# Performance work log

Hardware: AMD Instinct MI355X
Metric: run time of the kernel (lower is better)

The kernel has to match this reference:

```python
import jax, jax.numpy as jnp
import numpy as np

B, NQ, NK = 4, 2048, 2048
DQ = DK = DV = 512
H = 8
DS = DV // H  # 64


def _layernorm(x, g, b, eps=1e-5):
    m = jnp.mean(x, axis=-1, keepdims=True)
    v = jnp.var(x, axis=-1, keepdims=True)
    return (x - m) * jax.lax.rsqrt(v + eps) * g + b


def setup_inputs() -> dict:
    key = jax.random.key(0)
    ks = jax.random.split(key, 16)
    def lin(k, fan_in, fan_out):
        # torch nn.Linear default init: U(-1/sqrt(fan_in), 1/sqrt(fan_in))
        bound = 1.0 / np.sqrt(fan_in)
        k1, k2 = jax.random.split(k)
        W = jax.random.uniform(k1, (fan_in, fan_out), jnp.float32, -bound, bound)
        b = jax.random.uniform(k2, (fan_out,), jnp.float32, -bound, bound)
        return W, b
    Wq, bq = lin(ks[0], DQ, DV)
    Wk, bk = lin(ks[1], DK, DV)
    Wv, bv = lin(ks[2], DK, DV)
    W0, b0 = lin(ks[3], DV, DV)
    W1, b1 = lin(ks[4], DV, DV)
    # xavier_uniform for kp/vp of shape (1, DS): bound = sqrt(6/(1+DS))
    xb = np.sqrt(6.0 / (1 + DS))
    kp = jax.random.uniform(ks[5], (DS,), jnp.float32, -xb, xb)
    vp = jax.random.uniform(ks[6], (DS,), jnp.float32, -xb, xb)
    return {
        "Q": jax.random.normal(ks[7], (B, NQ, DQ), jnp.float32),
        "K": jax.random.normal(ks[8], (B, NK, DK), jnp.float32),
        "Kpos": jax.random.uniform(ks[9], (B, NQ, NK), jnp.float32),
        "Wq": Wq, "bq": bq, "Wk": Wk, "bk": bk, "Wv": Wv, "bv": bv,
        "kp": kp, "vp": vp,
        "W0": W0, "b0": b0, "W1": W1, "b1": b1,
        "g0": jnp.ones((DV,), jnp.float32), "be0": jnp.zeros((DV,), jnp.float32),
        "g1": jnp.ones((DV,), jnp.float32), "be1": jnp.zeros((DV,), jnp.float32),
    }


def reference(Q, K, Kpos, Wq, bq, Wk, bk, Wv, bv, kp, vp, W0, b0, W1, b1, g0, be0, g1, be1):
    Qp = Q @ Wq + bq                       # [B,NQ,DV]
    Kp = K @ Wk + bk                       # [B,NK,DV]
    Vp = K @ Wv + bv                       # [B,NK,DV]
    # head split (torch split/cat along batch == reshape to [B,N,H,DS])
    Qh = Qp.reshape(B, NQ, H, DS)
    Kh = Kp.reshape(B, NK, H, DS)
    Vh = Vp.reshape(B, NK, H, DS)
    scale = 1.0 / np.sqrt(DV)              # NOTE: original scales by sqrt(dim_V), not per-head dim
    scores = jnp.einsum('bqhd,bkhd->bhqk', Qh, Kh) * scale
    # ShawRE key bias: KE[b,h,q,k] = Kpos[b,q,k] * <Qh[b,q,h,:], kp>
    qkp = jnp.einsum('bqhd,d->bhq', Qh, kp)          # [B,H,NQ]
    scores = scores + Kpos[:, None, :, :] * qkp[:, :, :, None]
    A = jax.nn.softmax(scores, axis=-1)              # [B,H,NQ,NK]
    out = jnp.einsum('bhqk,bkhd->bqhd', A, Vh)       # [B,NQ,H,DS]
    # ShawRE value bias: VE[b,q,h,:] = (sum_k A*Kpos) * vp
    akp = jnp.einsum('bhqk,bqk->bhq', A, Kpos)       # [B,H,NQ]
    out = out + akp.transpose(0, 2, 1)[..., None] * vp
    O = (Qh + out).reshape(B, NQ, DV)
    O = _layernorm(O, g0, be0)
    resO = O
    O = jax.nn.relu(O @ W0 + b0)           # fc_o[0] with relu (numlayers=2)
    O = resO + jax.nn.relu(O @ W1 + b1)    # fc_o[-1] + residual
    O = _layernorm(O, g1, be1)
    return O
```

## Files before the change

kernel.cpp:

```cpp
#include <hip/hip_runtime.h>
#include <math.h>

#define Bx  4
#define NQx 2048
#define NKx 2048
#define Dx  512
#define Hx  8

typedef __attribute__((ext_vector_type(8))) __bf16 bf16x8;
typedef __attribute__((ext_vector_type(4))) float f32x4;
typedef __attribute__((ext_vector_type(16))) float f32x16;

typedef const __attribute__((address_space(1))) unsigned int* gas_ptr;
typedef __attribute__((address_space(3))) unsigned int* lds_ptr;

__device__ __forceinline__ void gload16(const void* g, void* l){
  __builtin_amdgcn_global_load_lds((gas_ptr)g, (lds_ptr)l, 16, 0, 0);
}

__device__ __forceinline__ unsigned short f2bf(float f){
  union { float f; unsigned int u; } v; v.f = f;
  unsigned int r = (v.u + 0x7FFFu + ((v.u >> 16) & 1u)) >> 16;
  return (unsigned short)r;
}
__device__ __forceinline__ float bf2f(unsigned short u){
  union { unsigned int u; float f; } v; v.u = ((unsigned int)u) << 16; return v.f;
}
__device__ __forceinline__ unsigned int cvtpk_bf16(float a, float b){
  unsigned int d;
  asm("v_cvt_pk_bf16_f32 %0, %1, %2" : "=v"(d) : "v"(a), "v"(b));
  return d;
}
__device__ __forceinline__ void plane32_swap(unsigned int& a, unsigned int& b){
  asm("v_permlane32_swap_b32 %0, %1" : "+v"(a), "+v"(b));
}
__device__ __forceinline__ float fexp2(float x){
  float d; asm("v_exp_f32 %0, %1" : "=v"(d) : "v"(x)); return d;
}
__device__ __forceinline__ float fmax3(float a, float b, float c){
  float d; asm("v_max3_f32 %0, %1, %2, %3" : "=v"(d) : "v"(a), "v"(b), "v"(c)); return d;
}

__global__ __launch_bounds__(256) void mab_wt(
    const float* __restrict__ Wq, const float* __restrict__ Wk, const float* __restrict__ Wv,
    const float* __restrict__ W0, const float* __restrict__ W1,
    unsigned short* __restrict__ Wt)
{
  __shared__ unsigned short T[64][72];
  const int z = blockIdx.z;
  const float* W = (z==0)?Wq:(z==1)?Wk:(z==2)?Wv:(z==3)?W0:W1;
  unsigned short* O = Wt + (size_t)z*512*512;
  const int k0 = blockIdx.x*64, n0 = blockIdx.y*64;
  const int tid = threadIdx.x;
  #pragma unroll
  for (int i=0;i<4;++i){
    int id = tid + i*256;
    int r = id>>4, c4 = id&15;
    float4 v = *(const float4*)(W + (size_t)(k0+r)*512 + n0 + c4*4);
    ushort4 o; o.x=f2bf(v.x); o.y=f2bf(v.y); o.z=f2bf(v.z); o.w=f2bf(v.w);
    *(ushort4*)&T[r][c4*4] = o;
  }
  __syncthreads();
  #pragma unroll
  for (int i=0;i<2;++i){
    int id = tid + i*256;
    int c = id>>3, r8 = id&7;
    union { unsigned short u[8]; uint4 v; } o;
    #pragma unroll
    for (int j=0;j<8;++j) o.u[j] = T[r8*8+j][c];
    *(uint4*)(O + (size_t)(n0+c)*512 + k0 + r8*8) = o.v;
  }
}

__global__ __launch_bounds__(256) void mab_vt(
    const unsigned short* __restrict__ Vp, unsigned short* __restrict__ Vpt)
{
  __shared__ unsigned short T[64][72];
  const int r0 = blockIdx.x*64;
  const int c0 = blockIdx.y*64;
  const int b  = blockIdx.z;
  const int tid = threadIdx.x;
  #pragma unroll
  for (int i=0;i<2;++i){
    int id = tid + i*256;
    int r = id>>3, c8 = id&7;
    *(uint4*)&T[r][c8*8] = *(const uint4*)(Vp + (size_t)(b*NKx + r0+r)*512 + c0 + c8*8);
  }
  __syncthreads();
  #pragma unroll
  for (int i=0;i<2;++i){
    int id = tid + i*256;
    int c = id>>3, r8 = id&7;
    union { unsigned short u[8]; uint4 v; } o;
    #pragma unroll
    for (int j=0;j<8;++j) o.u[j] = T[r8*8+j][c];
    *(uint4*)(Vpt + ((size_t)(b*512) + c0 + c)*NKx + r0 + r8*8) = o.v;
  }
}

__global__ __launch_bounds__(256) void mab_gemm_proj(
    const float* __restrict__ Qf, const float* __restrict__ Kf,
    const unsigned short* __restrict__ Wt,
    const float* __restrict__ bq, const float* __restrict__ bk, const float* __restrict__ bv,
    unsigned short* __restrict__ Cb, float kscale)
{
  __shared__ unsigned short As[128][64];
  __shared__ unsigned short Bs[128][64];
  const int z = blockIdx.z;
  const float* A = (z==0) ? Qf : Kf;
  const unsigned short* W = Wt + (size_t)z*512*512;
  const float* bias = (z==0)?bq:((z==1)?bk:bv);
  const float sc = (z==1) ? kscale : 1.0f;
  const int m0 = blockIdx.y*128, n0 = blockIdx.x*128;
  const int tid = threadIdx.x, w = tid>>6, lane = tid&63, g = lane>>4, q16 = lane&15;
  const int wr = w>>1, wc = w&1;

  f32x4 acc[4][4];
  #pragma unroll
  for (int m=0;m<4;++m)
    #pragma unroll
    for (int n=0;n<4;++n) acc[m][n] = (f32x4){0.f,0.f,0.f,0.f};

  float4 areg[8];
  #pragma unroll
  for (int i=0;i<8;++i){
    int id = i*256 + tid, row = id>>4, qc = id&15;
    areg[i] = *(const float4*)(A + (size_t)(m0+row)*512 + qc*4);
  }

  for (int k0 = 0; k0 < 512; k0 += 64){
    __syncthreads();
    #pragma unroll
    for (int i=0;i<8;++i){
      int id = i*256 + tid, row = id>>4, qc = id&15;
      unsigned int lo = cvtpk_bf16(areg[i].x, areg[i].y);
      unsigned int hi = cvtpk_bf16(areg[i].z, areg[i].w);
      unsigned int* dst = (unsigned int*)((char*)&As[0][0] + row*128
                          + ((qc>>1) ^ (row&7))*16 + (qc&1)*8);
      dst[0] = lo; dst[1] = hi;
    }
    #pragma unroll
    for (int i=0;i<4;++i){
      int o   = (w*4 + i)*1024 + lane*16;
      int row = o >> 7;
      int c   = (o >> 4) & 7;
      int cs  = c ^ (row & 7);
      gload16(W + (size_t)(n0+row)*512 + k0 + cs*8, (char*)&Bs[0][0] + (w*4+i)*1024);
    }
    __syncthreads();
    if (k0 + 64 < 512){
      #pragma unroll
      for (int i=0;i<8;++i){
        int id = i*256 + tid, row = id>>4, qc = id&15;
        areg[i] = *(const float4*)(A + (size_t)(m0+row)*512 + (k0+64) + qc*4);
      }
    }
    #pragma unroll
    for (int ks=0;ks<2;++ks){
      bf16x8 af[4], bfr[4];
      #pragma unroll
      for (int m=0;m<4;++m){
        int row = wr*64 + m*16 + q16;
        int c   = (ks*4 + g) ^ (row & 7);
        af[m] = *(const bf16x8*)((const char*)&As[0][0] + row*128 + c*16);
      }
      #pragma unroll
      for (int n=0;n<4;++n){
        int row = wc*64 + n*16 + q16;
        int c   = (ks*4 + g) ^ (row & 7);
        bfr[n] = *(const bf16x8*)((const char*)&Bs[0][0] + row*128 + c*16);
      }
      #pragma unroll
      for (int m=0;m<4;++m)
        #pragma unroll
        for (int n=0;n<4;++n)
          acc[m][n] = __builtin_amdgcn_mfma_f32_16x16x32_bf16(af[m], bfr[n], acc[m][n], 0,0,0);
    }
  }

  const size_t ZS = (size_t)8192*512;
  #pragma unroll
  for (int m=0;m<4;++m){
    const int rowl = wr*64 + m*16 + g*4;
    #pragma unroll
    for (int n=0;n<4;++n){
      const int col = n0 + wc*64 + n*16 + q16;
      const float bv2 = bias[col];
      #pragma unroll
      for (int r=0;r<4;++r){
        float v = (acc[m][n][r] + bv2) * sc;
        Cb[(size_t)z*ZS + (size_t)(m0 + rowl + r)*512 + col] = f2bf(v);
      }
    }
  }
}

__global__ __launch_bounds__(256) void mab_gemm_mfma(
    const unsigned short* __restrict__ A, const unsigned short* __restrict__ W,
    const float* __restrict__ bias, const float* __restrict__ res,
    unsigned short* __restrict__ Cb, float* __restrict__ Cf, int relu)
{
  __shared__ unsigned short As[128][64];
  __shared__ unsigned short Bs[128][64];
  const int m0 = blockIdx.y*128, n0 = blockIdx.x*128;
  const int tid = threadIdx.x, w = tid>>6, lane = tid&63, g = lane>>4, q16 = lane&15;
  const int wr = w>>1, wc = w&1;

  f32x4 acc[4][4];
  #pragma unroll
  for (int m=0;m<4;++m)
    #pragma unroll
    for (int n=0;n<4;++n) acc[m][n] = (f32x4){0.f,0.f,0.f,0.f};

  for (int k0 = 0; k0 < 512; k0 += 64){
    __syncthreads();
    #pragma unroll
    for (int i=0;i<4;++i){
      int o   = (w*4 + i)*1024 + lane*16;
      int row = o >> 7;
      int c   = (o >> 4) & 7;
      int cs  = c ^ (row & 7);
      gload16(A + (size_t)(m0+row)*512 + k0 + cs*8, (char*)&As[0][0] + (w*4+i)*1024);
      gload16(W + (size_t)(n0+row)*512 + k0 + cs*8, (char*)&Bs[0][0] + (w*4+i)*1024);
    }
    __syncthreads();
    #pragma unroll
    for (int ks=0;ks<2;++ks){
      bf16x8 af[4], bfr[4];
      #pragma unroll
      for (int m=0;m<4;++m){
        int row = wr*64 + m*16 + q16;
        int c   = (ks*4 + g) ^ (row & 7);
        af[m] = *(const bf16x8*)((const char*)&As[0][0] + row*128 + c*16);
      }
      #pragma unroll
      for (int n=0;n<4;++n){
        int row = wc*64 + n*16 + q16;
        int c   = (ks*4 + g) ^ (row & 7);
        bfr[n] = *(const bf16x8*)((const char*)&Bs[0][0] + row*128 + c*16);
      }
      #pragma unroll
      for (int m=0;m<4;++m)
        #pragma unroll
        for (int n=0;n<4;++n)
          acc[m][n] = __builtin_amdgcn_mfma_f32_16x16x32_bf16(af[m], bfr[n], acc[m][n], 0,0,0);
    }
  }

  #pragma unroll
  for (int m=0;m<4;++m){
    const int rowl = wr*64 + m*16 + g*4;
    #pragma unroll
    for (int n=0;n<4;++n){
      const int col = n0 + wc*64 + n*16 + q16;
      const float bv = bias[col];
      #pragma unroll
      for (int r=0;r<4;++r){
        float v = acc[m][n][r] + bv;
        if (relu) v = fmaxf(v, 0.f);
        size_t off = (size_t)(m0 + rowl + r)*512 + col;
        if (res) v += res[off];
        if (Cb) Cb[off] = f2bf(v);
        if (Cf) Cf[off] = v;
      }
    }
  }
}

__global__ __launch_bounds__(256) void mab_attn2(
    const unsigned short* __restrict__ Qp, const unsigned short* __restrict__ Kp,
    const unsigned short* __restrict__ Vpt,
    const float* __restrict__ Kpos, const float* __restrict__ kp, const float* __restrict__ vp,
    float* __restrict__ X)
{
  __shared__ unsigned short Kb[2][64][64];
  __shared__ unsigned short Vb[2][64][64];
  __shared__ unsigned short Qs[128][72];

  const int q0 = blockIdx.x*128;
  const int h  = blockIdx.y;
  const int b  = blockIdx.z;
  const int tid = threadIdx.x, w = tid>>6, lane = tid&63;
  const int q32 = lane & 31, hi = lane >> 5;

  const unsigned short* Qg = Qp + ((size_t)(b*NQx + q0))*Dx + h*64;
  const unsigned short* Kg = Kp + ((size_t)b*NKx)*Dx + h*64;
  const unsigned short* Vg = Vpt + ((size_t)(b*512) + h*64)*NKx;
  const float* KProw = Kpos + (size_t)b*NQx*NKx + (size_t)(q0 + w*32 + q32)*NKx;

  const int sr = lane>>3;
  const int sc = lane&7;

  #pragma unroll
  for (int i=0;i<2;++i){
    int r  = i*8 + sr;
    int cs = sc ^ (r & 7);
    gload16(Kg + (size_t)(w*16 + r)*Dx + cs*8, (char*)&Kb[0][0][0] + w*2048 + i*1024);
    gload16(Vg + (size_t)(w*16 + r)*NKx + cs*8, (char*)&Vb[0][0][0] + w*2048 + i*1024);
  }
  f32x4 kq[2][4];
  #pragma unroll
  for (int n=0;n<2;++n)
    #pragma unroll
    for (int a=0;a<4;++a)
      kq[n][a] = *(const f32x4*)(KProw + n*32 + a*8 + hi*4);
  #pragma unroll
  for (int i=0;i<4;++i){
    int id = tid + i*256;
    int r = id>>3, c8 = id&7;
    *(uint4*)&Qs[r][c8*8] = *(const uint4*)(Qg + (size_t)r*Dx + c8*8);
  }
  __syncthreads();

  bf16x8 qf[4];
  #pragma unroll
  for (int ds=0; ds<4; ++ds)
    qf[ds] = *(const bf16x8*)&Qs[w*32 + q32][ds*16 + hi*8];

  float qkp = 0.f;
  #pragma unroll
  for (int ds=0; ds<4; ++ds){
    union { bf16x8 v; unsigned short u[8]; } qa; qa.v = qf[ds];
    #pragma unroll
    for (int j=0;j<8;++j)
      qkp = fmaf(bf2f(qa.u[j]), kp[ds*16 + hi*8 + j], qkp);
  }
  qkp += __shfl_xor(qkp, 32);
  qkp *= 1.4426950408889634f;

  float m_i = -1e30f, l_i = 0.f, a_i = 0.f;
  f32x16 accT[2];
  #pragma unroll
  for (int db=0; db<2; ++db)
    #pragma unroll
    for (int r=0;r<16;++r) accT[db][r] = 0.f;

  const int NT = NKx/64;

  for (int kt = 0; kt < NT; ++kt){
    const int cur = kt & 1;
    const int k0 = kt*64;

    if (kt+1 < NT){
      const int k1 = k0 + 64;
      #pragma unroll
      for (int i=0;i<2;++i){
        int r  = i*8 + sr;
        int cs = sc ^ (r & 7);
        gload16(Kg + (size_t)(k1 + w*16 + r)*Dx + cs*8,
                (char*)&Kb[cur^1][0][0] + w*2048 + i*1024);
        gload16(Vg + (size_t)(w*16 + r)*NKx + k1 + cs*8,
                (char*)&Vb[cur^1][0][0] + w*2048 + i*1024);
      }
    }
    __builtin_amdgcn_sched_barrier(0);

    f32x16 sT[2];
    __builtin_amdgcn_s_setprio(1);
    #pragma unroll
    for (int n=0;n<2;++n){
      f32x16 c;
      #pragma unroll
      for (int r=0;r<16;++r) c[r] = 0.f;
      #pragma unroll
      for (int ds=0; ds<4; ++ds){
        int row = n*32 + q32;
        int cc  = (ds*2 + hi) ^ (q32 & 7);
        bf16x8 kf = *(const bf16x8*)((const char*)&Kb[cur][0][0] + row*128 + cc*16);
        c = __builtin_amdgcn_mfma_f32_32x32x16_bf16(kf, qf[ds], c, 0,0,0);
      }
      sT[n] = c;
    }
    __builtin_amdgcn_s_setprio(0);

    #pragma unroll
    for (int n=0;n<2;++n)
      #pragma unroll
      for (int r=0;r<16;++r)
        sT[n][r] = fmaf(kq[n][r>>2][r&3], qkp, sT[n][r]);

    float m0a = fmax3(sT[0][0], sT[0][1], sT[0][2]);
    float m0b = fmax3(sT[0][3], sT[0][4], sT[0][5]);
    float m0c = fmax3(sT[0][6], sT[0][7], sT[0][8]);
    float m0d = fmax3(sT[0][9], sT[0][10], sT[0][11]);
    float m0e = fmax3(sT[0][12], sT[0][13], sT[0][14]);
    float m1a = fmax3(sT[1][0], sT[1][1], sT[1][2]);
    float m1b = fmax3(sT[1][3], sT[1][4], sT[1][5]);
    float m1c = fmax3(sT[1][6], sT[1][7], sT[1][8]);
    float m1d = fmax3(sT[1][9], sT[1][10], sT[1][11]);
    float m1e = fmax3(sT[1][12], sT[1][13], sT[1][14]);
    float rm = fmax3(fmax3(m0a, m0b, m0c), fmax3(m0d, m0e, sT[0][15]),
                     fmax3(fmax3(m1a, m1b, m1c), fmax3(m1d, m1e, sT[1][15]), m_i));
    rm = fmaxf(rm, __shfl_xor(rm, 32));

    if (!__all(rm <= m_i + 11.544f)){
      float al = fexp2(m_i - rm);
      m_i = rm;
      l_i *= al; a_i *= al;
      #pragma unroll
      for (int db=0; db<2; ++db)
        #pragma unroll
        for (int r=0;r<16;++r) accT[db][r] *= al;
    }

    float ps = 0.f, pk = 0.f;
    #pragma unroll
    for (int n=0;n<2;++n)
      #pragma unroll
      for (int r=0;r<16;++r){
        float p = fexp2(sT[n][r] - m_i);
        sT[n][r] = p;
        ps += p;
        pk = fmaf(p, kq[n][r>>2][r&3], pk);
      }

    {
      const int kn = (kt+1 < NT) ? (k0 + 64) : k0;
      #pragma unroll
      for (int n=0;n<2;++n)
        #pragma unroll
        for (int a=0;a<4;++a)
          kq[n][a] = *(const f32x4*)(KProw + kn + n*32 + a*8 + hi*4);
    }

    ps += __shfl_xor(ps, 32);
    pk += __shfl_xor(pk, 32);
    l_i += ps; a_i += pk;

    union PW { unsigned int u[4]; bf16x8 v; } pa[4];
    #pragma unroll
    for (int n=0;n<2;++n){
      unsigned int w0 = cvtpk_bf16(sT[n][0],  sT[n][1]);
      unsigned int w1 = cvtpk_bf16(sT[n][2],  sT[n][3]);
      unsigned int w2 = cvtpk_bf16(sT[n][4],  sT[n][5]);
      unsigned int w3 = cvtpk_bf16(sT[n][6],  sT[n][7]);
      unsigned int w4 = cvtpk_bf16(sT[n][8],  sT[n][9]);
      unsigned int w5 = cvtpk_bf16(sT[n][10], sT[n][11]);
      unsigned int w6 = cvtpk_bf16(sT[n][12], sT[n][13]);
      unsigned int w7 = cvtpk_bf16(sT[n][14], sT[n][15]);
      plane32_swap(w0, w2);
      plane32_swap(w1, w3);
      plane32_swap(w4, w6);
      plane32_swap(w5, w7);
      pa[n*2+0].u[0]=w0; pa[n*2+0].u[1]=w1; pa[n*2+0].u[2]=w2; pa[n*2+0].u[3]=w3;
      pa[n*2+1].u[0]=w4; pa[n*2+1].u[1]=w5; pa[n*2+1].u[2]=w6; pa[n*2+1].u[3]=w7;
    }

    __builtin_amdgcn_s_setprio(1);
    #pragma unroll
    for (int st=0; st<4; ++st){
      #pragma unroll
      for (int db=0; db<2; ++db){
        int row = db*32 + q32;
        int cc  = (st*2 + hi) ^ (q32 & 7);
        bf16x8 vf = *(const bf16x8*)((const char*)&Vb[cur][0][0] + row*128 + cc*16);
        accT[db] = __builtin_amdgcn_mfma_f32_32x32x16_bf16(vf, pa[st].v, accT[db], 0,0,0);
      }
    }
    __builtin_amdgcn_s_setprio(0);

    asm volatile("s_waitcnt vmcnt(8)" ::: "memory");
    __builtin_amdgcn_s_barrier();
  }

  float inv = 1.0f / l_i;
  float aw  = a_i * inv;
  float* Xrow = X + ((size_t)(b*NQx + q0 + w*32 + q32))*Dx + h*64;
  #pragma unroll
  for (int db=0; db<2; ++db){
    #pragma unroll
    for (int a=0; a<4; ++a){
      int d0 = db*32 + a*8 + hi*4;
      f32x4 vpv = *(const f32x4*)(vp + d0);
      float4 o;
      o.x = fmaf(accT[db][a*4+0], inv, bf2f(Qs[w*32+q32][d0+0]) + aw*vpv[0]);
      o.y = fmaf(accT[db][a*4+1], inv, bf2f(Qs[w*32+q32][d0+1]) + aw*vpv[1]);
      o.z = fmaf(accT[db][a*4+2], inv, bf2f(Qs[w*32+q32][d0+2]) + aw*vpv[2]);
      o.w = fmaf(accT[db][a*4+3], inv, bf2f(Qs[w*32+q32][d0+3]) + aw*vpv[3]);
      *(float4*)(Xrow + d0) = o;
    }
  }
}

__global__ __launch_bounds__(256) void mab_ln2(
    const float* __restrict__ Xin, const float* __restrict__ g,
    const float* __restrict__ be, float* __restrict__ Yf, unsigned short* __restrict__ Yb)
{
  const int row = blockIdx.x;
  const int tid = threadIdx.x;
  const float* x = Xin + (size_t)row*Dx;
  float2 v = *(const float2*)(x + tid*2);
  float s  = v.x + v.y;
  float sq = fmaf(v.x,v.x, v.y*v.y);
  #pragma unroll
  for (int m=1; m<64; m<<=1){ s += __shfl_xor(s,m); sq += __shfl_xor(sq,m); }
  __shared__ float red[2][4];
  const int wid = tid>>6, lane = tid&63;
  if (lane==0){ red[0][wid]=s; red[1][wid]=sq; }
  __syncthreads();
  s  = red[0][0]+red[0][1]+red[0][2]+red[0][3];
  sq = red[1][0]+red[1][1]+red[1][2]+red[1][3];
  float mean = s*(1.0f/Dx);
  float var  = sq*(1.0f/Dx) - mean*mean;
  float rstd = rsqrtf(var + 1e-5f);
  float2 gg = *(const float2*)(g  + tid*2);
  float2 bb = *(const float2*)(be + tid*2);
  float2 o;
  o.x = (v.x-mean)*rstd*gg.x + bb.x;
  o.y = (v.y-mean)*rstd*gg.y + bb.y;
  if (Yf) *(float2*)(Yf + (size_t)row*Dx + tid*2) = o;
  if (Yb){
    ushort2 ob; ob.x = f2bf(o.x); ob.y = f2bf(o.y);
    *(ushort2*)(Yb + (size_t)row*Dx + tid*2) = ob;
  }
}

extern "C" void kernel_launch(void* const* d_in, const int* in_sizes, int n_in,
                              void* d_out, int out_size, void* d_ws, size_t ws_size,
                              hipStream_t stream)
{
  const float* Q    = (const float*)d_in[0];
  const float* K    = (const float*)d_in[1];
  const float* Kpos = (const float*)d_in[2];
  const float* Wq   = (const float*)d_in[3];
  const float* bq   = (const float*)d_in[4];
  const float* Wk   = (const float*)d_in[5];
  const float* bk   = (const float*)d_in[6];
  const float* Wv   = (const float*)d_in[7];
  const float* bv   = (const float*)d_in[8];
  const float* kp   = (const float*)d_in[9];
  const float* vp   = (const float*)d_in[10];
  const float* W0   = (const float*)d_in[11];
  const float* b0   = (const float*)d_in[12];
  const float* W1   = (const float*)d_in[13];
  const float* b1   = (const float*)d_in[14];
  const float* g0   = (const float*)d_in[15];
  const float* be0  = (const float*)d_in[16];
  const float* g1   = (const float*)d_in[17];
  const float* be1  = (const float*)d_in[18];
  float* out = (float*)d_out;
  char* wsb  = (char*)d_ws;

  const size_t MB = 1024*1024;
  unsigned short* Qp  = (unsigned short*)(wsb);
  unsigned short* Kp  = (unsigned short*)(wsb + 8*MB);
  unsigned short* Vp  = (unsigned short*)(wsb + 16*MB);
  float*          O0  = (float*)         (wsb + 24*MB);
  unsigned short* Vpt = (unsigned short*)(wsb + 40*MB);
  unsigned short* O0b = (unsigned short*)(wsb + 48*MB);
  unsigned short* Wt  = (unsigned short*)(wsb + 56*MB);
  unsigned short* T1  = Vp;

  const float kscale = 0.044194173824159216f * 1.4426950408889634f;

  mab_wt<<<dim3(8,8,5), 256, 0, stream>>>(Wq, Wk, Wv, W0, W1, Wt);
  mab_gemm_proj<<<dim3(4,64,3), 256, 0, stream>>>(Q, K, Wt, bq, bk, bv, Qp, kscale);
  mab_vt<<<dim3(32,8,4), 256, 0, stream>>>(Vp, Vpt);
  mab_attn2<<<dim3(16,8,4), 256, 0, stream>>>(Qp, Kp, Vpt, Kpos, kp, vp, out);
  mab_ln2<<<8192, 256, 0, stream>>>(out, g0, be0, O0, O0b);
  mab_gemm_mfma<<<dim3(4,64,1), 256, 0, stream>>>(
      O0b, Wt + (size_t)3*512*512, b0, nullptr, T1, nullptr, 1);
  mab_gemm_mfma<<<dim3(4,64,1), 256, 0, stream>>>(
      T1, Wt + (size_t)4*512*512, b1, O0, nullptr, out, 1);
  mab_ln2<<<8192, 256, 0, stream>>>(out, g1, be1, out, nullptr);
}
```

Before: 210.0 us.

## Split attention over key halves and merge partials inside the first layernorm

The attention kernel now splits the key range into two halves across the grid's z dimension, doubling the block count from 512 to 1024. Each block writes unnormalized bf16 partial outputs plus its running max, sum and Kpos-weighted sum. A new merge kernel combines the halves, adds the Q residual and vp bias, and applies the first layernorm, writing only bf16. Other changes: Q is read straight from global memory instead of through LDS, the Kpos loads move to the top of each iteration, occupancy is hinted at 4 blocks, and the residual is read back as bf16. This adds traffic for the partial results and the merge pass, and a bf16 residual loses precision.

```diff
diff --git a/kernel.cpp b/kernel.cpp
--- a/kernel.cpp
+++ b/kernel.cpp
@@ -197,7 +197,7 @@
 
 __global__ __launch_bounds__(256) void mab_gemm_mfma(
     const unsigned short* __restrict__ A, const unsigned short* __restrict__ W,
-    const float* __restrict__ bias, const float* __restrict__ res,
+    const float* __restrict__ bias, const unsigned short* __restrict__ resb,
     unsigned short* __restrict__ Cb, float* __restrict__ Cf, int relu)
 {
   __shared__ unsigned short As[128][64];
@@ -259,7 +259,7 @@
         float v = acc[m][n][r] + bv;
         if (relu) v = fmaxf(v, 0.f);
         size_t off = (size_t)(m0 + rowl + r)*512 + col;
-        if (res) v += res[off];
+        if (resb) v += bf2f(resb[off]);
         if (Cb) Cb[off] = f2bf(v);
         if (Cf) Cf[off] = v;
       }
@@ -267,23 +267,23 @@
   }
 }
 
-__global__ __launch_bounds__(256) void mab_attn2(
+__global__ __launch_bounds__(256, 4) void mab_attn6(
     const unsigned short* __restrict__ Qp, const unsigned short* __restrict__ Kp,
     const unsigned short* __restrict__ Vpt,
-    const float* __restrict__ Kpos, const float* __restrict__ kp, const float* __restrict__ vp,
-    float* __restrict__ X)
+    const float* __restrict__ Kpos, const float* __restrict__ kp,
+    unsigned short* __restrict__ OP, float4* __restrict__ MLA)
 {
   __shared__ unsigned short Kb[2][64][64];
   __shared__ unsigned short Vb[2][64][64];
-  __shared__ unsigned short Qs[128][72];
 
   const int q0 = blockIdx.x*128;
   const int h  = blockIdx.y;
-  const int b  = blockIdx.z;
+  const int b  = blockIdx.z >> 1;
+  const int zz = blockIdx.z & 1;
   const int tid = threadIdx.x, w = tid>>6, lane = tid&63;
   const int q32 = lane & 31, hi = lane >> 5;
-
-  const unsigned short* Qg = Qp + ((size_t)(b*NQx + q0))*Dx + h*64;
+  const int kbase = zz*1024;
+
   const unsigned short* Kg = Kp + ((size_t)b*NKx)*Dx + h*64;
   const unsigned short* Vg = Vpt + ((size_t)(b*512) + h*64)*NKx;
   const float* KProw = Kpos + (size_t)b*NQx*NKx + (size_t)(q0 + w*32 + q32)*NKx;
@@ -293,29 +293,17 @@
 
   #pragma unroll
   for (int i=0;i<2;++i){
-    int r  = i*8 + sr;
+    int r  = w*16 + i*8 + sr;
     int cs = sc ^ (r & 7);
-    gload16(Kg + (size_t)(w*16 + r)*Dx + cs*8, (char*)&Kb[0][0][0] + w*2048 + i*1024);
-    gload16(Vg + (size_t)(w*16 + r)*NKx + cs*8, (char*)&Vb[0][0][0] + w*2048 + i*1024);
-  }
-  f32x4 kq[2][4];
-  #pragma unroll
-  for (int n=0;n<2;++n)
-    #pragma unroll
-    for (int a=0;a<4;++a)
-      kq[n][a] = *(const f32x4*)(KProw + n*32 + a*8 + hi*4);
-  #pragma unroll
-  for (int i=0;i<4;++i){
-    int id = tid + i*256;
-    int r = id>>3, c8 = id&7;
-    *(uint4*)&Qs[r][c8*8] = *(const uint4*)(Qg + (size_t)r*Dx + c8*8);
-  }
-  __syncthreads();
-
+    gload16(Kg + (size_t)(kbase + r)*Dx + cs*8, (char*)&Kb[0][0][0] + w*2048 + i*1024);
+    gload16(Vg + (size_t)r*NKx + kbase + cs*8, (char*)&Vb[0][0][0] + w*2048 + i*1024);
+  }
+
+  const unsigned short* Qrowp = Qp + ((size_t)(b*NQx + q0 + w*32 + q32))*Dx + h*64;
   bf16x8 qf[4];
   #pragma unroll
   for (int ds=0; ds<4; ++ds)
-    qf[ds] = *(const bf16x8*)&Qs[w*32 + q32][ds*16 + hi*8];
+    qf[ds] = *(const bf16x8*)(Qrowp + ds*16 + hi*8);
 
   float qkp = 0.f;
   #pragma unroll
@@ -335,21 +323,28 @@
     #pragma unroll
     for (int r=0;r<16;++r) accT[db][r] = 0.f;
 
-  const int NT = NKx/64;
-
-  for (int kt = 0; kt < NT; ++kt){
-    const int cur = kt & 1;
-    const int k0 = kt*64;
-
-    if (kt+1 < NT){
+  __syncthreads();
+
+  for (int t = 0; t < 16; ++t){
+    const int cur = t & 1;
+    const int k0 = kbase + t*64;
+
+    f32x4 kq[2][4];
+    #pragma unroll
+    for (int n=0;n<2;++n)
+      #pragma unroll
+      for (int a=0;a<4;++a)
+        kq[n][a] = *(const f32x4*)(KProw + k0 + n*32 + a*8 + hi*4);
+
+    if (t+1 < 16){
       const int k1 = k0 + 64;
       #pragma unroll
       for (int i=0;i<2;++i){
-        int r  = i*8 + sr;
+        int r  = w*16 + i*8 + sr;
         int cs = sc ^ (r & 7);
-        gload16(Kg + (size_t)(k1 + w*16 + r)*Dx + cs*8,
+        gload16(Kg + (size_t)(k1 + r)*Dx + cs*8,
                 (char*)&Kb[cur^1][0][0] + w*2048 + i*1024);
-        gload16(Vg + (size_t)(w*16 + r)*NKx + k1 + cs*8,
+        gload16(Vg + (size_t)r*NKx + k1 + cs*8,
                 (char*)&Vb[cur^1][0][0] + w*2048 + i*1024);
       }
     }
@@ -413,16 +408,6 @@
         ps += p;
         pk = fmaf(p, kq[n][r>>2][r&3], pk);
       }
-
-    {
-      const int kn = (kt+1 < NT) ? (k0 + 64) : k0;
-      #pragma unroll
-      for (int n=0;n<2;++n)
-        #pragma unroll
-        for (int a=0;a<4;++a)
-          kq[n][a] = *(const f32x4*)(KProw + kn + n*32 + a*8 + hi*4);
-    }
-
     ps += __shfl_xor(ps, 32);
     pk += __shfl_xor(pk, 32);
     l_i += ps; a_i += pk;
@@ -459,32 +444,80 @@
     }
     __builtin_amdgcn_s_setprio(0);
 
-    asm volatile("s_waitcnt vmcnt(8)" ::: "memory");
-    __builtin_amdgcn_s_barrier();
-  }
-
-  float inv = 1.0f / l_i;
-  float aw  = a_i * inv;
-  float* Xrow = X + ((size_t)(b*NQx + q0 + w*32 + q32))*Dx + h*64;
+    __syncthreads();
+  }
+
+  const size_t rowg = (size_t)(b*NQx + q0 + w*32 + q32);
+  unsigned short* Orow = OP + (size_t)zz*(8192*512) + rowg*Dx + h*64;
   #pragma unroll
   for (int db=0; db<2; ++db){
     #pragma unroll
-    for (int a=0; a<4; ++a){
-      int d0 = db*32 + a*8 + hi*4;
-      f32x4 vpv = *(const f32x4*)(vp + d0);
-      float4 o;
-      o.x = fmaf(accT[db][a*4+0], inv, bf2f(Qs[w*32+q32][d0+0]) + aw*vpv[0]);
-      o.y = fmaf(accT[db][a*4+1], inv, bf2f(Qs[w*32+q32][d0+1]) + aw*vpv[1]);
-      o.z = fmaf(accT[db][a*4+2], inv, bf2f(Qs[w*32+q32][d0+2]) + aw*vpv[2]);
-      o.w = fmaf(accT[db][a*4+3], inv, bf2f(Qs[w*32+q32][d0+3]) + aw*vpv[3]);
-      *(float4*)(Xrow + d0) = o;
-    }
-  }
+    for (int a2=0; a2<4; ++a2){
+      int d0 = db*32 + a2*8 + hi*4;
+      uint2 pk2;
+      pk2.x = cvtpk_bf16(accT[db][a2*4+0], accT[db][a2*4+1]);
+      pk2.y = cvtpk_bf16(accT[db][a2*4+2], accT[db][a2*4+3]);
+      *(uint2*)(Orow + d0) = pk2;
+    }
+  }
+  if (hi == 0){
+    float4 mla; mla.x = m_i; mla.y = l_i; mla.z = a_i; mla.w = 0.f;
+    MLA[(size_t)zz*65536 + rowg*8 + h] = mla;
+  }
+}
+
+__global__ __launch_bounds__(256) void mab_merge_ln(
+    const unsigned short* __restrict__ OP, const float4* __restrict__ MLA,
+    const unsigned short* __restrict__ Qp, const float* __restrict__ vp,
+    const float* __restrict__ g, const float* __restrict__ be,
+    unsigned short* __restrict__ Yb)
+{
+  const int row = blockIdx.x;
+  const int tid = threadIdx.x;
+  const int h = tid >> 5;
+  const size_t R = (size_t)8192*512;
+
+  float4 A0 = MLA[(size_t)row*8 + h];
+  float4 A1 = MLA[65536 + (size_t)row*8 + h];
+  float mM  = fmaxf(A0.x, A1.x);
+  float al0 = fexp2(A0.x - mM), al1 = fexp2(A1.x - mM);
+  float l   = fmaf(al0, A0.y, al1*A1.y);
+  float inv = 1.0f / l;
+  float aw  = fmaf(al0, A0.z, al1*A1.z) * inv;
+
+  const int d = tid*2;
+  ushort2 o0 = *(const ushort2*)(OP + (size_t)row*Dx + d);
+  ushort2 o1 = *(const ushort2*)(OP + R + (size_t)row*Dx + d);
+  ushort2 qh = *(const ushort2*)(Qp + (size_t)row*Dx + d);
+  float2 vv  = *(const float2*)(vp + (d & 63));
+  float2 v;
+  v.x = fmaf(fmaf(al0, bf2f(o0.x), al1*bf2f(o1.x)), inv, bf2f(qh.x) + aw*vv.x);
+  v.y = fmaf(fmaf(al0, bf2f(o0.y), al1*bf2f(o1.y)), inv, bf2f(qh.y) + aw*vv.y);
+
+  float s  = v.x + v.y;
+  float sq = fmaf(v.x,v.x, v.y*v.y);
+  #pragma unroll
+  for (int m=1; m<64; m<<=1){ s += __shfl_xor(s,m); sq += __shfl_xor(sq,m); }
+  __shared__ float red[2][4];
+  const int wid = tid>>6, lane = tid&63;
+  if (lane==0){ red[0][wid]=s; red[1][wid]=sq; }
+  __syncthreads();
+  s  = red[0][0]+red[0][1]+red[0][2]+red[0][3];
+  sq = red[1][0]+red[1][1]+red[1][2]+red[1][3];
+  float mean = s*(1.0f/Dx);
+  float var  = sq*(1.0f/Dx) - mean*mean;
+  float rstd = rsqrtf(var + 1e-5f);
+  float2 gg = *(const float2*)(g  + d);
+  float2 bb = *(const float2*)(be + d);
+  ushort2 ob;
+  ob.x = f2bf((v.x-mean)*rstd*gg.x + bb.x);
+  ob.y = f2bf((v.y-mean)*rstd*gg.y + bb.y);
+  *(ushort2*)(Yb + (size_t)row*Dx + d) = ob;
 }
 
 __global__ __launch_bounds__(256) void mab_ln2(
     const float* __restrict__ Xin, const float* __restrict__ g,
-    const float* __restrict__ be, float* __restrict__ Yf, unsigned short* __restrict__ Yb)
+    const float* __restrict__ be, float* __restrict__ Yf)
 {
   const int row = blockIdx.x;
   const int tid = threadIdx.x;
@@ -508,11 +541,7 @@
   float2 o;
   o.x = (v.x-mean)*rstd*gg.x + bb.x;
   o.y = (v.y-mean)*rstd*gg.y + bb.y;
-  if (Yf) *(float2*)(Yf + (size_t)row*Dx + tid*2) = o;
-  if (Yb){
-    ushort2 ob; ob.x = f2bf(o.x); ob.y = f2bf(o.y);
-    *(ushort2*)(Yb + (size_t)row*Dx + tid*2) = ob;
-  }
+  *(float2*)(Yf + (size_t)row*Dx + tid*2) = o;
 }
 
 extern "C" void kernel_launch(void* const* d_in, const int* in_sizes, int n_in,
@@ -545,10 +574,11 @@
   unsigned short* Qp  = (unsigned short*)(wsb);
   unsigned short* Kp  = (unsigned short*)(wsb + 8*MB);
   unsigned short* Vp  = (unsigned short*)(wsb + 16*MB);
-  float*          O0  = (float*)         (wsb + 24*MB);
-  unsigned short* Vpt = (unsigned short*)(wsb + 40*MB);
-  unsigned short* O0b = (unsigned short*)(wsb + 48*MB);
-  unsigned short* Wt  = (unsigned short*)(wsb + 56*MB);
+  unsigned short* Vpt = (unsigned short*)(wsb + 24*MB);
+  unsigned short* OP  = (unsigned short*)(wsb + 32*MB);
+  float4*         MLA = (float4*)        (wsb + 48*MB);
+  unsigned short* Wt  = (unsigned short*)(wsb + 50*MB);
+  unsigned short* O0b = Vpt;
   unsigned short* T1  = Vp;
 
   const float kscale = 0.044194173824159216f * 1.4426950408889634f;
@@ -556,11 +586,11 @@
   mab_wt<<<dim3(8,8,5), 256, 0, stream>>>(Wq, Wk, Wv, W0, W1, Wt);
   mab_gemm_proj<<<dim3(4,64,3), 256, 0, stream>>>(Q, K, Wt, bq, bk, bv, Qp, kscale);
   mab_vt<<<dim3(32,8,4), 256, 0, stream>>>(Vp, Vpt);
-  mab_attn2<<<dim3(16,8,4), 256, 0, stream>>>(Qp, Kp, Vpt, Kpos, kp, vp, out);
-  mab_ln2<<<8192, 256, 0, stream>>>(out, g0, be0, O0, O0b);
+  mab_attn6<<<dim3(16,8,8), 256, 0, stream>>>(Qp, Kp, Vpt, Kpos, kp, OP, MLA);
+  mab_merge_ln<<<8192, 256, 0, stream>>>(OP, MLA, Qp, vp, g0, be0, O0b);
   mab_gemm_mfma<<<dim3(4,64,1), 256, 0, stream>>>(
       O0b, Wt + (size_t)3*512*512, b0, nullptr, T1, nullptr, 1);
   mab_gemm_mfma<<<dim3(4,64,1), 256, 0, stream>>>(
-      T1, Wt + (size_t)4*512*512, b1, O0, nullptr, out, 1);
-  mab_ln2<<<8192, 256, 0, stream>>>(out, g1, be1, out, nullptr);
-}
+      T1, Wt + (size_t)4*512*512, b1, O0b, nullptr, out, 1);
+  mab_ln2<<<8192, 256, 0, stream>>>(out, g1, be1, out);
+}
```

Result: slower. 254.0 us (+21.0%).
